# Performance work log

Hardware: AMD Instinct MI355X
Metric: run time of the kernel (lower is better)

Reference implementation:

```python
import jax, jax.numpy as jnp
import numpy as np

SEQ, BATCH = 1024, 2
N_HEAD, D_MODEL = 16, 1024
Q_LORA, KV_LORA = 20, 20
ROPE = D_MODEL // N_HEAD // 2   # 32 qk_rope_head_dim
NOPE = D_MODEL // N_HEAD // 2   # 32 qk_nope_head_dim
V_DIM = D_MODEL // N_HEAD       # 64
N_EXP, HID = 4, 1024            # hidden_dim = d_inner//5 = 5120//5
N_GROUP, TOPK_GROUP, TOP_K = 2, 2, 1
ROUTED_SCALE = 1.0


def setup_inputs() -> dict:
    key = jax.random.key(0)
    ks = jax.random.split(key, 16)
    sc = 0.02
    return {
        'dec_inp': jax.random.normal(ks[0], (SEQ, BATCH, D_MODEL), jnp.float32),
        'wq_a': jax.random.normal(ks[1], (D_MODEL, Q_LORA), jnp.float32) * sc,
        'q_norm_w': jnp.ones((Q_LORA,), jnp.float32),
        'wq_b': jax.random.normal(ks[2], (Q_LORA, N_HEAD * (NOPE + ROPE)), jnp.float32) * sc,
        'wkv_a': jax.random.normal(ks[3], (D_MODEL, KV_LORA + ROPE), jnp.float32) * sc,
        'kv_norm_w': jnp.ones((KV_LORA,), jnp.float32),
        'wkv_b': jax.random.normal(ks[4], (KV_LORA, N_HEAD * (NOPE + V_DIM)), jnp.float32) * sc,
        'wo': jax.random.normal(ks[5], (N_HEAD * V_DIM, D_MODEL), jnp.float32) * sc,
        'gate_w': jax.random.normal(ks[6], (N_EXP, D_MODEL), jnp.float32) * sc,
        'exp_gate': jax.random.normal(ks[7], (N_EXP, D_MODEL, HID), jnp.float32) * sc,
        'exp_up': jax.random.normal(ks[8], (N_EXP, D_MODEL, HID), jnp.float32) * sc,
        'exp_down': jax.random.normal(ks[9], (N_EXP, HID, D_MODEL), jnp.float32) * sc,
        'sh_gate': jax.random.normal(ks[10], (D_MODEL, HID), jnp.float32) * sc,
        'sh_up': jax.random.normal(ks[11], (D_MODEL, HID), jnp.float32) * sc,
        'sh_down': jax.random.normal(ks[12], (HID, D_MODEL), jnp.float32) * sc,
    }


def _rms(x, w, eps=1e-6):
    return x * jax.lax.rsqrt(jnp.mean(x * x, axis=-1, keepdims=True) + eps) * w


def _freqs(seqlen):
    # precompute_freqs_cis(rope_dim * n_head, seqlen): dim = 512 here
    dim = ROPE * N_HEAD
    inv = 1.0 / (10000.0 ** (jnp.arange(0, dim, 2, dtype=jnp.float32) / dim))  # [dim//2]
    ang = jnp.arange(seqlen, dtype=jnp.float32)[:, None] * inv[None, :]       # [s, dim//2]
    ang = ang.reshape(seqlen, N_HEAD, ROPE // 2)
    return jnp.cos(ang), jnp.sin(ang)


def _rope(x, cos, sin):
    # x: [b, s, h, ROPE]; interleaved-pair complex rotation
    b, s, h, _ = x.shape
    xr = x.reshape(b, s, h, ROPE // 2, 2)
    x0, x1 = xr[..., 0], xr[..., 1]
    c = cos[None]  # [1, s, h, ROPE//2]
    sn = sin[None]
    o0 = x0 * c - x1 * sn
    o1 = x0 * sn + x1 * c
    return jnp.stack([o0, o1], axis=-1).reshape(b, s, h, ROPE)


def reference(dec_inp, wq_a, q_norm_w, wq_b, wkv_a, kv_norm_w, wkv_b, wo,
              gate_w, exp_gate, exp_up, exp_down, sh_gate, sh_up, sh_down):
    x = jnp.swapaxes(dec_inp, 0, 1)  # [b, s, d]
    b, s, d = x.shape
    # ---- MLA attention ----
    q = _rms(x @ wq_a, q_norm_w) @ wq_b                       # [b, s, h*(nope+rope)]
    q = q.reshape(b, s, N_HEAD, NOPE + ROPE)
    q_nope, q_pe = q[..., :NOPE], q[..., NOPE:]
    kv = x @ wkv_a                                            # [b, s, kv_lora+rope]
    ckv, k_pe = kv[..., :KV_LORA], kv[..., KV_LORA:]
    kvb = (_rms(ckv, kv_norm_w) @ wkv_b).reshape(b, s, N_HEAD, NOPE + V_DIM)
    k_nope, v = kvb[..., :NOPE], kvb[..., NOPE:]
    cos, sin = _freqs(s)
    q_pe = _rope(q_pe, cos, sin)
    k_pe_h = _rope(jnp.broadcast_to(k_pe[:, :, None, :], (b, s, N_HEAD, ROPE)), cos, sin)
    qf = jnp.concatenate([q_nope, q_pe], axis=-1)             # [b, s, h, 64]
    kf = jnp.concatenate([k_nope, k_pe_h], axis=-1)
    scale = 1.0 / np.sqrt(NOPE + ROPE)
    scores = jnp.einsum('bshd,bthd->bhst', qf, kf) * scale    # mask=None in the source forward
    probs = jax.nn.softmax(scores, axis=-1)
    attn = jnp.einsum('bhst,bthd->bshd', probs, v).reshape(b, s, N_HEAD * V_DIM)
    y = attn @ wo                                             # [b, s, d]
    y = jnp.swapaxes(y, 0, 1)                                 # [s, b, d]
    # ---- DeepSeekMoE (group_limited_greedy, top_k=1, 1 shared expert) ----
    xf = y.reshape(-1, d)                                     # [T, d]
    T = xf.shape[0]
    sc = jax.nn.softmax(xf @ gate_w.T, axis=-1)               # [T, E]
    gsc = sc.reshape(T, N_GROUP, N_EXP // N_GROUP).max(axis=-1)  # [T, n_group]
    _, gidx = jax.lax.top_k(gsc, TOPK_GROUP)
    gmask = jax.nn.one_hot(gidx, N_GROUP, dtype=sc.dtype).sum(axis=1)  # [T, n_group]
    smask = jnp.repeat(gmask, N_EXP // N_GROUP, axis=-1)      # [T, E]
    tw, ti = jax.lax.top_k(jnp.where(smask > 0, sc, 0.0), TOP_K)
    comb = (jax.nn.one_hot(ti, N_EXP, dtype=sc.dtype) * tw[..., None]).sum(axis=1) * ROUTED_SCALE  # [T, E]
    g = jnp.einsum('td,edh->teh', xf, exp_gate)
    u = jnp.einsum('td,edh->teh', xf, exp_up)
    dn = jnp.einsum('teh,ehd->ted', jax.nn.silu(g) * u, exp_down)
    routed = jnp.einsum('ted,te->td', dn, comb)
    shared = (jax.nn.silu(xf @ sh_gate) * (xf @ sh_up)) @ sh_down
    return (routed + shared).reshape(s, b, d)
```

## Files before the change

kernel.cpp:

```cpp
#include <hip/hip_runtime.h>
#include <hip/hip_bf16.h>
#include <math.h>

#define SEQ 1024
#define BATCH 2
#define T 2048
#define DM 1024
#define NH 16
#define NOPE 32
#define HD 64
#define QL 20
#define KVL 20
#define KVA 52
#define HID 1024
#define NEXP 4
#define LSTR 80

typedef short bf16x8 __attribute__((ext_vector_type(8)));
typedef float f32x4 __attribute__((ext_vector_type(4)));
typedef float f32x16 __attribute__((ext_vector_type(16)));
typedef __hip_bfloat16 bf16;

static __device__ __forceinline__ float sigmoidf_(float x) {
    return 1.0f / (1.0f + __expf(-x));
}
static __device__ __forceinline__ unsigned short bfbits(float x) {
    bf16 h = __float2bfloat16(x);
    return *reinterpret_cast<unsigned short*>(&h);
}
static __device__ __forceinline__ unsigned cvt_pk_bf16(float lo, float hi) {
    unsigned r;
    asm("v_cvt_pk_bf16_f32 %0, %1, %2" : "=v"(r) : "v"(lo), "v"(hi));
    return r;
}
static __device__ __forceinline__ void gload16(const bf16* g, char* l) {
    __builtin_amdgcn_global_load_lds(
        (const __attribute__((address_space(1))) unsigned int*)g,
        (__attribute__((address_space(3))) unsigned int*)l, 16, 0, 0);
}
static __device__ __forceinline__ void barrier_() {
    asm volatile("" ::: "memory");
    __builtin_amdgcn_s_barrier();
    asm volatile("" ::: "memory");
}
#define VMWAIT(N) asm volatile("s_waitcnt vmcnt(" #N ")" ::: "memory")

__global__ __launch_bounds__(256) void k_setup(
    const float* __restrict__ wo, const float* __restrict__ sg,
    const float* __restrict__ su, const float* __restrict__ sd,
    const float* __restrict__ eg, const float* __restrict__ eu,
    const float* __restrict__ ed,
    bf16* __restrict__ woT, bf16* __restrict__ sgT, bf16* __restrict__ suT,
    bf16* __restrict__ sdT, bf16* __restrict__ egT, bf16* __restrict__ euT,
    bf16* __restrict__ edT,
    const float* __restrict__ wq_a, const float* __restrict__ wkv_a,
    const float* __restrict__ wq_b, const float* __restrict__ wkv_b,
    bf16* __restrict__ loraT, bf16* __restrict__ wqbT, bf16* __restrict__ wkvbT,
    float* __restrict__ ctab, float* __restrict__ stab)
{
    int z = blockIdx.z;
    int tid = threadIdx.x;
    if (z < 16) {
        __shared__ float tile[32][33];
        const float* in; bf16* out;
        if      (z == 0) { in = wo; out = woT; }
        else if (z == 1) { in = sg; out = sgT; }
        else if (z == 2) { in = su; out = suT; }
        else if (z == 3) { in = sd; out = sdT; }
        else if (z < 8)  { size_t o = (size_t)(z - 4)  * DM * HID; in = eg + o; out = egT + o; }
        else if (z < 12) { size_t o = (size_t)(z - 8)  * DM * HID; in = eu + o; out = euT + o; }
        else             { size_t o = (size_t)(z - 12) * HID * DM; in = ed + o; out = edT + o; }
        int c0 = blockIdx.x * 32, r0 = blockIdx.y * 32;
        int tx = tid & 31, ty = tid >> 5;
        #pragma unroll
        for (int ii = 0; ii < 4; ++ii)
            tile[ty + ii * 8][tx] = in[(size_t)(r0 + ty + ii * 8) * 1024 + c0 + tx];
        __syncthreads();
        int c = tid >> 3, rg = (tid & 7) * 4;
        ushort4 o4;
        o4.x = bfbits(tile[rg + 0][c]);
        o4.y = bfbits(tile[rg + 1][c]);
        o4.z = bfbits(tile[rg + 2][c]);
        o4.w = bfbits(tile[rg + 3][c]);
        *(ushort4*)&out[(size_t)(c0 + c) * 1024 + r0 + rg] = o4;
    } else if (z == 16) {
        int s = blockIdx.y * 32 + blockIdx.x;
        int p = tid;
        float freq = exp2f(-(float)p * (13.287712379549449f / 256.0f));
        float ang = (float)s * freq;
        float sn, cs;
        __sincosf(ang, &sn, &cs);
        ctab[s * 256 + p] = cs;
        stab[s * 256 + p] = sn;
    } else {
        int idx = (blockIdx.y * 32 + blockIdx.x) * 256 + tid;
        if (z == 17) {
            if (idx >= 80 * 1024) return;
            int n = idx >> 10, k = idx & 1023;
            float v = (n < 20) ? wq_a[k * QL + n] : (n < 72 ? wkv_a[k * KVA + (n - 20)] : 0.f);
            loraT[idx] = __float2bfloat16(v);
        } else if (z == 18) {
            if (idx >= 1024 * 32) return;
            int n = idx >> 5, k = idx & 31;
            wqbT[idx] = __float2bfloat16(k < 20 ? wq_b[k * DM + n] : 0.f);
        } else {
            if (idx >= 1536 * 32) return;
            int n = idx >> 5, k = idx & 31;
            wkvbT[idx] = __float2bfloat16(k < 20 ? wkv_b[k * (NH * 96) + n] : 0.f);
        }
    }
}

__global__ __launch_bounds__(256) void k_p1(
    const float* __restrict__ dec, const bf16* __restrict__ loraT,
    float* __restrict__ lora4)
{
    __shared__ __align__(16) char As[128 * LSTR];
    __shared__ __align__(16) char Bs[80 * LSTR];
    const int tid = threadIdx.x;
    const int kz = blockIdx.x;
    const int m0 = blockIdx.y * 128;
    const int lane = tid & 63, wave = tid >> 6;
    const int g = lane >> 4, c = lane & 15;
    f32x4 acc[2][5] = {};
    for (int ks = 0; ks < 16; ++ks) {
        int k0 = kz * 512 + ks * 32;
        __syncthreads();
        #pragma unroll
        for (int pass = 0; pass < 4; ++pass) {
            int row = (tid >> 3) + pass * 32;
            int t = m0 + row;
            int b = t >> 10, s = t & 1023;
            f32x4 v = *(const f32x4*)&dec[(size_t)(s * 2 + b) * DM + k0 + (tid & 7) * 4];
            ushort4 h4;
            h4.x = bfbits(v[0]); h4.y = bfbits(v[1]);
            h4.z = bfbits(v[2]); h4.w = bfbits(v[3]);
            *(ushort4*)&As[row * LSTR + (tid & 7) * 8] = h4;
        }
        if (tid < 160) {
            int row = tid >> 1, hf = tid & 1;
            const bf16* src = &loraT[row * 1024 + k0 + hf * 16];
            *(int4*)&Bs[row * LSTR + hf * 32]      = *(const int4*)&src[0];
            *(int4*)&Bs[row * LSTR + hf * 32 + 16] = *(const int4*)&src[8];
        }
        __syncthreads();
        bf16x8 af[2], bff[5];
        #pragma unroll
        for (int mi = 0; mi < 2; ++mi)
            af[mi] = *(const bf16x8*)&As[(wave * 32 + mi * 16 + c) * LSTR + 16 * g];
        #pragma unroll
        for (int nf = 0; nf < 5; ++nf)
            bff[nf] = *(const bf16x8*)&Bs[(nf * 16 + c) * LSTR + 16 * g];
        #pragma unroll
        for (int mi = 0; mi < 2; ++mi)
            #pragma unroll
            for (int nf = 0; nf < 5; ++nf)
                acc[mi][nf] = __builtin_amdgcn_mfma_f32_16x16x32_bf16(af[mi], bff[nf], acc[mi][nf], 0, 0, 0);
    }
    #pragma unroll
    for (int mi = 0; mi < 2; ++mi)
        #pragma unroll
        for (int nf = 0; nf < 5; ++nf)
            #pragma unroll
            for (int r = 0; r < 4; ++r) {
                int col = nf * 16 + c;
                if (col < 72) {
                    int row = m0 + wave * 32 + mi * 16 + 4 * g + r;
                    lora4[((size_t)kz * T + row) * 72 + col] = acc[mi][nf][r];
                }
            }
}

__global__ __launch_bounds__(256) void k_p2m(
    const float* __restrict__ lora4, const float* __restrict__ qnw,
    const float* __restrict__ kvnw, const float* __restrict__ ctab,
    const float* __restrict__ stab, bf16* __restrict__ nrmq,
    bf16* __restrict__ nrmkv, bf16* __restrict__ kb, int* __restrict__ cnt)
{
    int bid = blockIdx.x, tid = threadIdx.x;
    if (bid == 0 && tid < 16) cnt[tid] = 0;
    {
        int t = bid, p = tid;
        int r = p & 15, h = p >> 4, s = t & (SEQ - 1);
        float y0 = lora4[t * 72 + 40 + 2 * r] + lora4[(size_t)(T + t) * 72 + 40 + 2 * r];
        float y1 = lora4[t * 72 + 41 + 2 * r] + lora4[(size_t)(T + t) * 72 + 41 + 2 * r];
        float cs = ctab[s * 256 + p], sn = stab[s * 256 + p];
        ushort2 pk;
        pk.x = bfbits(y0 * cs - y1 * sn);
        pk.y = bfbits(y0 * sn + y1 * cs);
        *(ushort2*)&kb[(size_t)t * DM + h * HD + NOPE + 2 * r] = pk;
    }
    if (bid < 8) {
        int t = bid * 256 + tid;
        float lq[20], lk[20];
        float ssq = 0.f, ssk = 0.f;
        #pragma unroll
        for (int i = 0; i < 20; ++i) {
            lq[i] = lora4[t * 72 + i] + lora4[(size_t)(T + t) * 72 + i];
            ssq += lq[i] * lq[i];
        }
        #pragma unroll
        for (int i = 0; i < 20; ++i) {
            lk[i] = lora4[t * 72 + 20 + i] + lora4[(size_t)(T + t) * 72 + 20 + i];
            ssk += lk[i] * lk[i];
        }
        float fq = rsqrtf(ssq / 20.f + 1e-6f);
        float fk = rsqrtf(ssk / 20.f + 1e-6f);
        #pragma unroll
        for (int i = 0; i < 32; ++i) {
            nrmq[t * 32 + i]  = __float2bfloat16(i < 20 ? lq[i] * fq * qnw[i]  : 0.f);
            nrmkv[t * 32 + i] = __float2bfloat16(i < 20 ? lk[i] * fk * kvnw[i] : 0.f);
        }
    }
}

__global__ __launch_bounds__(256) void k_p3(
    const bf16* __restrict__ nrmq, const bf16* __restrict__ wqbT,
    const bf16* __restrict__ nrmkv, const bf16* __restrict__ wkvbT,
    const float* __restrict__ ctab, const float* __restrict__ stab,
    bf16* __restrict__ qb, bf16* __restrict__ kb, bf16* __restrict__ vt_g)
{
    const int zq = (blockIdx.z == 0);
    if (zq && blockIdx.x >= 16) return;
    __shared__ __align__(16) char As[128 * LSTR];
    __shared__ __align__(16) char Bs[64 * LSTR];
    const int tid = threadIdx.x;
    const int m0 = blockIdx.y * 128, n0 = blockIdx.x * 64;
    const int lane = tid & 63, wave = tid >> 6;
    const int g = lane >> 4, c = lane & 15;
    const int wm = wave >> 1, wn = wave & 1;
    const bf16* nrm = zq ? nrmq : nrmkv;
    const bf16* wT  = zq ? wqbT : wkvbT;
    {
        int row = tid >> 1, hf = tid & 1;
        const bf16* sa = &nrm[(size_t)(m0 + row) * 32 + hf * 16];
        *(int4*)&As[row * LSTR + hf * 32]      = *(const int4*)&sa[0];
        *(int4*)&As[row * LSTR + hf * 32 + 16] = *(const int4*)&sa[8];
        int brow = tid >> 2;
        *(int4*)&Bs[brow * LSTR + (tid & 3) * 16] = *(const int4*)&wT[(size_t)(n0 + brow) * 32 + (tid & 3) * 8];
    }
    __syncthreads();
    f32x4 acc[4][2] = {};
    bf16x8 af[4], bfr[2];
    #pragma unroll
    for (int mi = 0; mi < 4; ++mi)
        af[mi] = *(const bf16x8*)&As[(wm * 64 + mi * 16 + c) * LSTR + 16 * g];
    #pragma unroll
    for (int ni = 0; ni < 2; ++ni)
        bfr[ni] = *(const bf16x8*)&Bs[(wn * 32 + ni * 16 + c) * LSTR + 16 * g];
    #pragma unroll
    for (int mi = 0; mi < 4; ++mi)
        #pragma unroll
        for (int ni = 0; ni < 2; ++ni)
            acc[mi][ni] = __builtin_amdgcn_mfma_f32_16x16x32_bf16(af[mi], bfr[ni], acc[mi][ni], 0, 0, 0);

    if (zq) {
        #pragma unroll
        for (int mi = 0; mi < 4; ++mi)
            #pragma unroll
            for (int ni = 0; ni < 2; ++ni) {
                #pragma unroll
                for (int r = 0; r < 4; ++r) acc[mi][ni][r] *= 0.18033688f;
                int n = n0 + wn * 32 + ni * 16 + c;
                int w = n & 63;
                if (w < 32) {
                    #pragma unroll
                    for (int r = 0; r < 4; ++r) {
                        int row = m0 + wm * 64 + mi * 16 + 4 * g + r;
                        qb[(size_t)row * DM + n] = __float2bfloat16(acc[mi][ni][r]);
                    }
                } else {
                    int h = n >> 6;
                    int pidx = h * 16 + ((w - 32) >> 1);
                    int odd = w & 1;
                    #pragma unroll
                    for (int r = 0; r < 4; ++r) {
                        int row = m0 + wm * 64 + mi * 16 + 4 * g + r;
                        int s = row & (SEQ - 1);
                        float own = acc[mi][ni][r];
                        float oth = __shfl_xor(own, 1);
                        float cs = ctab[s * 256 + pidx], sn = stab[s * 256 + pidx];
                        float o = odd ? (oth * sn + own * cs) : (own * cs - oth * sn);
                        qb[(size_t)row * DM + n] = __float2bfloat16(o);
                    }
                }
            }
    } else {
        #pragma unroll
        for (int mi = 0; mi < 4; ++mi)
            #pragma unroll
            for (int ni = 0; ni < 2; ++ni) {
                int n = n0 + wn * 32 + ni * 16 + c;
                int h = n / 96, w = n - h * 96;
                int row0 = m0 + wm * 64 + mi * 16 + 4 * g;
                if (w < NOPE) {
                    #pragma unroll
                    for (int r = 0; r < 4; ++r)
                        kb[(size_t)(row0 + r) * DM + h * HD + w] = __float2bfloat16(acc[mi][ni][r]);
                } else {
                    int d = w - NOPE;
                    int b = row0 >> 10, s0 = row0 & (SEQ - 1);
                    ushort4 v4;
                    v4.x = bfbits(acc[mi][ni][0]);
                    v4.y = bfbits(acc[mi][ni][1]);
                    v4.z = bfbits(acc[mi][ni][2]);
                    v4.w = bfbits(acc[mi][ni][3]);
                    *(ushort4*)&vt_g[(((size_t)(b * NH + h) * HD + d) << 10) + s0] = v4;
                }
            }
    }
}

__global__ __launch_bounds__(512) void k_attn(
    const bf16* __restrict__ qb, const bf16* __restrict__ kb,
    const bf16* __restrict__ vt_g, bf16* __restrict__ ab)
{
    __shared__ __align__(16) char stage[2][16384];
    __shared__ float pol[4][32][65];
    __shared__ float mll[4][32][2];

    const int orig = blockIdx.y * 8 + blockIdx.x;
    const int h  = (orig & 7) * 2 + ((orig >> 3) & 1);
    const int qt = orig >> 4;
    const int b = blockIdx.z;
    const int tid = threadIdx.x;
    const int lane = tid & 63, wave = tid >> 6;
    const int l31 = lane & 31, hi = lane >> 5;
    const int sp = wave >> 2, wq = wave & 3;
    const int q0 = qt * 128 + wq * 32;
    char* ks = stage[sp];
    char* vt = stage[sp] + 8192;
    const int ptid = tid & 255;

    bf16x8 qf[4];
    {
        const bf16* qrow = &qb[(size_t)(b * SEQ + q0 + l31) * DM + h * HD + 8 * hi];
        #pragma unroll
        for (int st = 0; st < 4; ++st)
            qf[st] = *(const bf16x8*)&qrow[16 * st];
    }

    f32x16 o0 = {}, o1 = {};
    float m_run = -3.0e38f, l_run = 0.f;
    const size_t vbase = ((size_t)(b * NH + h) * HD) << 10;

    for (int ktl = 0; ktl < 8; ++ktl) {
        const int kt = sp * 8 + ktl;
        __syncthreads();
        #pragma unroll
        for (int ps = 0; ps < 2; ++ps) {
            int row = (ptid >> 3) + ps * 32;
            int col8 = (ptid & 7) * 8;
            int sw = (col8 * 2) ^ ((row & 7) << 4);
            int4 kv4 = *(const int4*)&kb[(size_t)(b * SEQ + kt * 64 + row) * DM + h * HD + col8];
            *(int4*)&ks[row * 128 + sw] = kv4;
            int4 vv4 = *(const int4*)&vt_g[vbase + ((size_t)row << 10) + kt * 64 + col8];
            *(int4*)&vt[row * 128 + sw] = vv4;
        }
        __syncthreads();

        f32x16 sc0 = {}, sc1 = {};
        #pragma unroll
        for (int st = 0; st < 4; ++st) {
            int colb = 32 * st + 16 * hi;
            int r0 = l31;
            bf16x8 kf0 = *(const bf16x8*)&ks[r0 * 128 + (colb ^ ((r0 & 7) << 4))];
            sc0 = __builtin_amdgcn_mfma_f32_32x32x16_bf16(kf0, qf[st], sc0, 0, 0, 0);
            int r1 = 32 + l31;
            bf16x8 kf1 = *(const bf16x8*)&ks[r1 * 128 + (colb ^ ((r1 & 7) << 4))];
            sc1 = __builtin_amdgcn_mfma_f32_32x32x16_bf16(kf1, qf[st], sc1, 0, 0, 0);
        }

        float mt = fmaxf(sc0[0], sc1[0]);
        #pragma unroll
        for (int i = 1; i < 16; ++i) mt = fmaxf(mt, fmaxf(sc0[i], sc1[i]));
        mt = fmaxf(mt, __shfl_xor(mt, 32));

        if (!__all(mt <= m_run + 8.0f)) {
            float m_new = fmaxf(m_run, mt);
            float corr = exp2f(m_run - m_new);
            m_run = m_new;
            l_run *= corr;
            #pragma unroll
            for (int i = 0; i < 16; ++i) { o0[i] *= corr; o1[i] *= corr; }
        }
        float ls = 0.f;
        #pragma unroll
        for (int i = 0; i < 16; ++i) {
            sc0[i] = exp2f(sc0[i] - m_run);
            sc1[i] = exp2f(sc1[i] - m_run);
            ls += sc0[i] + sc1[i];
        }
        ls += __shfl_xor(ls, 32);
        l_run += ls;

        unsigned pk0[8], pk1[8];
        #pragma unroll
        for (int i = 0; i < 8; ++i) {
            pk0[i] = cvt_pk_bf16(sc0[2 * i], sc0[2 * i + 1]);
            pk1[i] = cvt_pk_bf16(sc1[2 * i], sc1[2 * i + 1]);
        }

#define PV_SUB(PK, KK)                                                          \
        {                                                                       \
            _Pragma("unroll")                                                   \
            for (int s = 0; s < 2; ++s) {                                       \
                unsigned sx = hi ? PK[4*s]   : PK[4*s+2];                       \
                unsigned rx = __shfl_xor(sx, 32);                               \
                unsigned sy = hi ? PK[4*s+1] : PK[4*s+3];                       \
                unsigned ry = __shfl_xor(sy, 32);                               \
                int4 bi;                                                        \
                bi.x = hi ? (int)rx : (int)PK[4*s];                             \
                bi.y = hi ? (int)ry : (int)PK[4*s+1];                           \
                bi.z = hi ? (int)PK[4*s+2] : (int)rx;                           \
                bi.w = hi ? (int)PK[4*s+3] : (int)ry;                           \
                bf16x8 bfr = *(bf16x8*)&bi;                                     \
                int cb = (KK) * 64 + 32 * s + 16 * hi;                          \
                {                                                               \
                    int vr = l31;                                               \
                    bf16x8 vf = *(const bf16x8*)&vt[vr * 128 + (cb ^ ((vr & 7) << 4))]; \
                    o0 = __builtin_amdgcn_mfma_f32_32x32x16_bf16(vf, bfr, o0, 0, 0, 0); \
                }                                                               \
                {                                                               \
                    int vr = 32 + l31;                                          \
                    bf16x8 vf = *(const bf16x8*)&vt[vr * 128 + (cb ^ ((vr & 7) << 4))]; \
                    o1 = __builtin_amdgcn_mfma_f32_32x32x16_bf16(vf, bfr, o1, 0, 0, 0); \
                }                                                               \
            }                                                                   \
        }
        PV_SUB(pk0, 0)
        PV_SUB(pk1, 1)
#undef PV_SUB
    }

    if (sp == 1) {
        #pragma unroll
        for (int i = 0; i < 16; ++i) {
            int d = (i & 3) + 8 * (i >> 2) + 4 * hi;
            pol[wq][l31][d]      = o0[i];
            pol[wq][l31][32 + d] = o1[i];
        }
        if (hi == 0) { mll[wq][l31][0] = m_run; mll[wq][l31][1] = l_run; }
    }
    __syncthreads();
    if (sp == 1) return;

    float m_b = mll[wq][l31][0], l_b = mll[wq][l31][1];
    float M = fmaxf(m_run, m_b);
    float wa = exp2f(m_run - M), wb = exp2f(m_b - M);
    float inv = 1.0f / (l_run * wa + l_b * wb);
    #pragma unroll
    for (int i = 0; i < 16; ++i) {
        int d = (i & 3) + 8 * (i >> 2) + 4 * hi;
        o0[i] = (o0[i] * wa + pol[wq][l31][d]      * wb) * inv;
        o1[i] = (o1[i] * wa + pol[wq][l31][32 + d] * wb) * inv;
    }

    char* tb = stage[0] + wq * 8192;
    #pragma unroll
    for (int i = 0; i < 8; ++i) {
        int dbase = 2 * (i & 1) + 8 * (i >> 1) + 4 * hi;
        *(unsigned*)&tb[l31 * 140 + (dbase) * 2]      = cvt_pk_bf16(o0[2 * i], o0[2 * i + 1]);
        *(unsigned*)&tb[l31 * 140 + (32 + dbase) * 2] = cvt_pk_bf16(o1[2 * i], o1[2 * i + 1]);
    }
    __builtin_amdgcn_s_waitcnt(0);
    #pragma unroll
    for (int p = 0; p < 8; ++p) {
        int idx = p * 64 + lane;
        int q = idx >> 4, c8 = idx & 15;
        int2 rv;
        rv.x = *(const int*)&tb[q * 140 + c8 * 8];
        rv.y = *(const int*)&tb[q * 140 + c8 * 8 + 4];
        *(int2*)&ab[(size_t)(b * SEQ + q0 + q) * DM + h * HD + c8 * 4] = rv;
    }
}

__global__ __launch_bounds__(512) void k_mm_plain(
    const bf16* __restrict__ A, const bf16* __restrict__ Bt, bf16* __restrict__ C)
{
    __shared__ __align__(16) char As[2][8192];
    __shared__ __align__(16) char Bs[2][4096];
    const int tid = threadIdx.x;
    const int lane = tid & 63, wave = tid >> 6;
    const int g = lane >> 4, c = lane & 15;
    const int wm = wave >> 1, wn = wave & 1;
    int orig = blockIdx.y * 16 + blockIdx.x;
    int swz = (orig & 7) * 32 + (orig >> 3);
    const int n0 = (swz & 15) * 64, m0 = (swz >> 4) * 128;

    const int ldr = lane >> 2;
    const int ldc = (lane & 3) * 8;
    const bf16* agp = &A[(size_t)(m0 + wave * 16 + ldr) * DM + ldc];
    const bool doB = wave >= 4;
    const bf16* bgp = &Bt[(size_t)(n0 + (wave & 3) * 16 + ldr) * DM + ldc];
    const int aoffL = wave * 1024, boffL = (wave & 3) * 1024;

    f32x4 acc[2][2] = {};
    const int NT = DM / 32;
    gload16(agp, As[0] + aoffL);
    if (doB) gload16(bgp, Bs[0] + boffL);
    for (int k = 0; k < NT; ++k) {
        const int cur = k & 1;
        if (k + 1 < NT) {
            gload16(agp + (k + 1) * 32, As[cur ^ 1] + aoffL);
            if (doB) gload16(bgp + (k + 1) * 32, Bs[cur ^ 1] + boffL);
            if (doB) VMWAIT(2); else VMWAIT(1);
        } else {
            VMWAIT(0);
        }
        barrier_();
        bf16x8 af[2], bfx[2];
        #pragma unroll
        for (int mi = 0; mi < 2; ++mi)
            af[mi] = *(const bf16x8*)&As[cur][(wm * 32 + mi * 16 + c) * 64 + g * 16];
        #pragma unroll
        for (int ni = 0; ni < 2; ++ni)
            bfx[ni] = *(const bf16x8*)&Bs[cur][(wn * 32 + ni * 16 + c) * 64 + g * 16];
        #pragma unroll
        for (int mi = 0; mi < 2; ++mi)
            #pragma unroll
            for (int ni = 0; ni < 2; ++ni)
                acc[mi][ni] = __builtin_amdgcn_mfma_f32_16x16x32_bf16(af[mi], bfx[ni], acc[mi][ni], 0, 0, 0);
        barrier_();
    }
    #pragma unroll
    for (int mi = 0; mi < 2; ++mi)
        #pragma unroll
        for (int ni = 0; ni < 2; ++ni)
            #pragma unroll
            for (int r = 0; r < 4; ++r)
                C[(size_t)(m0 + wm * 32 + mi * 16 + 4 * g + r) * DM + n0 + wn * 32 + ni * 16 + c]
                    = __float2bfloat16(acc[mi][ni][r]);
}

__global__ __launch_bounds__(512) void k_mm_gu_all(
    const bf16* __restrict__ X, const bf16* __restrict__ egT,
    const bf16* __restrict__ euT, const bf16* __restrict__ sgT,
    const bf16* __restrict__ suT, const int* __restrict__ cnt,
    const int* __restrict__ lists, bf16* __restrict__ act_r,
    bf16* __restrict__ act_s)
{
    const int e = blockIdx.z;
    const bool SH = (e == 4);
    const int ntok = SH ? T : cnt[e];
    int orig = blockIdx.y * 16 + blockIdx.x;
    int swz = (orig & 7) * 32 + (orig >> 3);
    const int n0 = (swz & 15) * 64, m0 = (swz >> 4) * 128;
    if (m0 >= ntok) return;
    __shared__ __align__(16) char As[2][8192];
    __shared__ __align__(16) char Bg[2][4096];
    __shared__ __align__(16) char Bu[2][4096];
    __shared__ int rowid[128];
    const int tid = threadIdx.x;
    if (tid < 128) {
        int idx = m0 + tid;
        rowid[tid] = SH ? idx : lists[e * T + (idx < ntok ? idx : ntok - 1)];
    }
    __syncthreads();
    const int lane = tid & 63, wave = tid >> 6;
    const int g = lane >> 4, c = lane & 15;
    const int wm = wave >> 1, wn = wave & 1;
    const bf16* Bge = SH ? sgT : egT + (size_t)e * HID * DM;
    const bf16* Bue = SH ? suT : euT + (size_t)e * HID * DM;
    bf16* act = SH ? act_s : act_r;

    const int ldr = lane >> 2;
    const int ldc = (lane & 3) * 8;
    const int myTok = rowid[wave * 16 + ldr];
    const bf16* agp = &X[(size_t)myTok * DM + ldc];
    const bool isG = wave < 4;
    const bf16* bgp = (isG ? Bge : Bue) + (size_t)(n0 + (wave & 3) * 16 + ldr) * DM + ldc;
    const int aoffL = wave * 1024, boffL = (wave & 3) * 1024;

    f32x4 accg[2][2] = {}, accu[2][2] = {};
    const int NT = DM / 32;
    gload16(agp, As[0] + aoffL);
    gload16(bgp, (isG ? Bg[0] : Bu[0]) + boffL);
    for (int k = 0; k < NT; ++k) {
        const int cur = k & 1;
        if (k + 1 < NT) {
            gload16(agp + (k + 1) * 32, As[cur ^ 1] + aoffL);
            gload16(bgp + (k + 1) * 32, (isG ? Bg[cur ^ 1] : Bu[cur ^ 1]) + boffL);
            VMWAIT(2);
        } else {
            VMWAIT(0);
        }
        barrier_();
        bf16x8 af[2], gf[2], uf[2];
        #pragma unroll
        for (int mi = 0; mi < 2; ++mi)
            af[mi] = *(const bf16x8*)&As[cur][(wm * 32 + mi * 16 + c) * 64 + g * 16];
        #pragma unroll
        for (int ni = 0; ni < 2; ++ni) {
            gf[ni] = *(const bf16x8*)&Bg[cur][(wn * 32 + ni * 16 + c) * 64 + g * 16];
            uf[ni] = *(const bf16x8*)&Bu[cur][(wn * 32 + ni * 16 + c) * 64 + g * 16];
        }
        #pragma unroll
        for (int mi = 0; mi < 2; ++mi)
            #pragma unroll
            for (int ni = 0; ni < 2; ++ni) {
                accg[mi][ni] = __builtin_amdgcn_mfma_f32_16x16x32_bf16(af[mi], gf[ni], accg[mi][ni], 0, 0, 0);
                accu[mi][ni] = __builtin_amdgcn_mfma_f32_16x16x32_bf16(af[mi], uf[ni], accu[mi][ni], 0, 0, 0);
            }
        barrier_();
    }
    #pragma unroll
    for (int mi = 0; mi < 2; ++mi)
        #pragma unroll
        for (int ni = 0; ni < 2; ++ni)
            #pragma unroll
            for (int r = 0; r < 4; ++r) {
                int lr = wm * 32 + mi * 16 + 4 * g + r;
                if (!SH && m0 + lr >= ntok) continue;
                int token = rowid[lr];
                float gv = accg[mi][ni][r], uv = accu[mi][ni][r];
                act[(size_t)token * HID + n0 + wn * 32 + ni * 16 + c] =
                    __float2bfloat16(gv * sigmoidf_(gv) * uv);
            }
}

__global__ __launch_bounds__(512) void k_mm_down_f(
    const bf16* __restrict__ Xr, const bf16* __restrict__ Xs,
    const bf16* __restrict__ edT, const bf16* __restrict__ sdT,
    const int* __restrict__ cnt, const int* __restrict__ lists,
    const float* __restrict__ wtok, float* __restrict__ out)
{
    const int e = blockIdx.z;
    const int ntok = cnt[e];
    int orig = blockIdx.y * 16 + blockIdx.x;
    int swz = (orig & 7) * 32 + (orig >> 3);
    const int n0 = (swz & 15) * 64, m0 = (swz >> 4) * 128;
    if (m0 >= ntok) return;
    __shared__ __align__(16) char Ar[2][8192];
    __shared__ __align__(16) char Az[2][8192];
    __shared__ __align__(16) char Br[2][4096];
    __shared__ __align__(16) char Bz[2][4096];
    __shared__ int rowid[128];
    const int tid = threadIdx.x;
    if (tid < 128) {
        int idx = m0 + tid;
        rowid[tid] = lists[e * T + (idx < ntok ? idx : ntok - 1)];
    }
    __syncthreads();
    const int lane = tid & 63, wave = tid >> 6;
    const int g = lane >> 4, c = lane & 15;
    const int wm = wave >> 1, wn = wave & 1;
    const bf16* Bde = edT + (size_t)e * HID * DM;

    const int ldr = lane >> 2;
    const int ldc = (lane & 3) * 8;
    const int myTok = rowid[wave * 16 + ldr];
    const bf16* agr = &Xr[(size_t)myTok * HID + ldc];
    const bf16* ags = &Xs[(size_t)myTok * HID + ldc];
    const bool isR = wave < 4;
    const bf16* bgp = (isR ? Bde : sdT) + (size_t)(n0 + (wave & 3) * 16 + ldr) * HID + ldc;
    const int aoffL = wave * 1024, boffL = (wave & 3) * 1024;

    f32x4 accr[2][2] = {}, accs[2][2] = {};
    const int NT = HID / 32;
    gload16(agr, Ar[0] + aoffL);
    gload16(ags, Az[0] + aoffL);
    gload16(bgp, (isR ? Br[0] : Bz[0]) + boffL);
    for (int k = 0; k < NT; ++k) {
        const int cur = k & 1;
        if (k + 1 < NT) {
            gload16(agr + (k + 1) * 32, Ar[cur ^ 1] + aoffL);
            gload16(ags + (k + 1) * 32, Az[cur ^ 1] + aoffL);
            gload16(bgp + (k + 1) * 32, (isR ? Br[cur ^ 1] : Bz[cur ^ 1]) + boffL);
            VMWAIT(3);
        } else {
            VMWAIT(0);
        }
        barrier_();
        bf16x8 afr[2], afs[2], bfr[2], bfs[2];
        #pragma unroll
        for (int mi = 0; mi < 2; ++mi) {
            afr[mi] = *(const bf16x8*)&Ar[cur][(wm * 32 + mi * 16 + c) * 64 + g * 16];
            afs[mi] = *(const bf16x8*)&Az[cur][(wm * 32 + mi * 16 + c) * 64 + g * 16];
        }
        #pragma unroll
        for (int ni = 0; ni < 2; ++ni) {
            bfr[ni] = *(const bf16x8*)&Br[cur][(wn * 32 + ni * 16 + c) * 64 + g * 16];
            bfs[ni] = *(const bf16x8*)&Bz[cur][(wn * 32 + ni * 16 + c) * 64 + g * 16];
        }
        #pragma unroll
        for (int mi = 0; mi < 2; ++mi)
            #pragma unroll
            for (int ni = 0; ni < 2; ++ni) {
                accr[mi][ni] = __builtin_amdgcn_mfma_f32_16x16x32_bf16(afr[mi], bfr[ni], accr[mi][ni], 0, 0, 0);
                accs[mi][ni] = __builtin_amdgcn_mfma_f32_16x16x32_bf16(afs[mi], bfs[ni], accs[mi][ni], 0, 0, 0);
            }
        barrier_();
    }
    #pragma unroll
    for (int mi = 0; mi < 2; ++mi)
        #pragma unroll
        for (int ni = 0; ni < 2; ++ni)
            #pragma unroll
            for (int r = 0; r < 4; ++r) {
                int lr = wm * 32 + mi * 16 + 4 * g + r;
                if (m0 + lr >= ntok) continue;
                int token = rowid[lr];
                int bt = token >> 10, st = token & (SEQ - 1);
                size_t oo = (size_t)st * (BATCH * DM) + bt * DM + n0 + wn * 32 + ni * 16 + c;
                out[oo] = accr[mi][ni][r] * wtok[token] + accs[mi][ni][r];
            }
}

__global__ __launch_bounds__(256) void k_gate(
    const bf16* __restrict__ y, const float* __restrict__ gw,
    int* __restrict__ cnt, int* __restrict__ lists, float* __restrict__ wtok)
{
    int warp = threadIdx.x >> 6, lane = threadIdx.x & 63;
    int t = blockIdx.x * 4 + warp;
    float acc[NEXP] = {};
    for (int d = lane; d < DM; d += 64) {
        float xv = __bfloat162float(y[(size_t)t * DM + d]);
        #pragma unroll
        for (int e = 0; e < NEXP; ++e) acc[e] += xv * gw[e * DM + d];
    }
    #pragma unroll
    for (int off = 32; off; off >>= 1)
        #pragma unroll
        for (int e = 0; e < NEXP; ++e) acc[e] += __shfl_xor(acc[e], off);
    if (lane == 0) {
        float mx = fmaxf(fmaxf(acc[0], acc[1]), fmaxf(acc[2], acc[3]));
        float ex[NEXP], ssum = 0.f;
        #pragma unroll
        for (int e = 0; e < NEXP; ++e) { ex[e] = __expf(acc[e] - mx); ssum += ex[e]; }
        int best = 0; float bv = ex[0];
        #pragma unroll
        for (int e = 1; e < NEXP; ++e) if (ex[e] > bv) { bv = ex[e]; best = e; }
        wtok[t] = bv / ssum;
        int pos = atomicAdd(&cnt[best], 1);
        lists[best * T + pos] = t;
    }
}

extern "C" void kernel_launch(void* const* d_in, const int* in_sizes, int n_in,
                              void* d_out, int out_size, void* d_ws, size_t ws_size,
                              hipStream_t stream) {
    (void)in_sizes; (void)n_in; (void)out_size; (void)ws_size;
    const float* dec      = (const float*)d_in[0];
    const float* wq_a     = (const float*)d_in[1];
    const float* q_norm_w = (const float*)d_in[2];
    const float* wq_b     = (const float*)d_in[3];
    const float* wkv_a    = (const float*)d_in[4];
    const float* kv_norm_w= (const float*)d_in[5];
    const float* wkv_b    = (const float*)d_in[6];
    const float* wo       = (const float*)d_in[7];
    const float* gate_w   = (const float*)d_in[8];
    const float* exp_gate = (const float*)d_in[9];
    const float* exp_up   = (const float*)d_in[10];
    const float* exp_down = (const float*)d_in[11];
    const float* sh_gate  = (const float*)d_in[12];
    const float* sh_up    = (const float*)d_in[13];
    const float* sh_down  = (const float*)d_in[14];
    float* out = (float*)d_out;

    char* W = (char*)d_ws;
    bf16* qb   = (bf16*)(W);
    bf16* kb   = (bf16*)(W + (4ull  << 20));
    bf16* vt_g = (bf16*)(W + (8ull  << 20));
    char* SMALL = W + (12ull << 20);
    bf16* ab   = (bf16*)(W + (12ull << 20));
    bf16* woT = (bf16*)(W + (16ull << 20));
    bf16* sgT = (bf16*)(W + (18ull << 20));
    bf16* suT = (bf16*)(W + (20ull << 20));
    bf16* sdT = (bf16*)(W + (22ull << 20));
    bf16* egT = (bf16*)(W + (24ull << 20));
    bf16* euT = (bf16*)(W + (32ull << 20));
    bf16* edT = (bf16*)(W + (40ull << 20));
    int*   cnt   = (int*)(W + (48ull << 20));
    int*   lists = cnt + 16;
    float* wtok  = (float*)(lists + NEXP * T);
    bf16* yb    = qb;
    bf16* act_r = kb;
    bf16* act_s = vt_g;

    float* lora4 = (float*)(SMALL);
    bf16*  loraT = (bf16*) (SMALL + 1179648);
    bf16*  wqbT  = (bf16*) (SMALL + 1343488);
    bf16*  wkvbT = (bf16*) (SMALL + 1409024);
    bf16*  nrmq  = (bf16*) (SMALL + 1507328);
    bf16*  nrmkv = (bf16*) (SMALL + 1638400);
    float* ctab  = (float*)(SMALL + 1769472);
    float* stab  = (float*)(SMALL + 2818048);

    k_setup<<<dim3(32, 32, 20), 256, 0, stream>>>(
        wo, sh_gate, sh_up, sh_down, exp_gate, exp_up, exp_down,
        woT, sgT, suT, sdT, egT, euT, edT,
        wq_a, wkv_a, wq_b, wkv_b, loraT, wqbT, wkvbT, ctab, stab);

    k_p1<<<dim3(2, 16), 256, 0, stream>>>(dec, loraT, lora4);
    k_p2m<<<T, 256, 0, stream>>>(lora4, q_norm_w, kv_norm_w, ctab, stab,
                                 nrmq, nrmkv, kb, cnt);
    k_p3<<<dim3(24, 16, 2), 256, 0, stream>>>(nrmq, wqbT, nrmkv, wkvbT,
                                              ctab, stab, qb, kb, vt_g);

    k_attn<<<dim3(8, 16, BATCH), 512, 0, stream>>>(qb, kb, vt_g, ab);
    k_mm_plain<<<dim3(16, 16), 512, 0, stream>>>(ab, woT, yb);
    k_gate<<<T / 4, 256, 0, stream>>>(yb, gate_w, cnt, lists, wtok);
    k_mm_gu_all<<<dim3(16, 16, NEXP + 1), 512, 0, stream>>>(
        yb, egT, euT, sgT, suT, cnt, lists, act_r, act_s);
    k_mm_down_f<<<dim3(16, 16, NEXP), 512, 0, stream>>>(
        act_r, act_s, edT, sdT, cnt, lists, wtok, out);
}
```

Baseline: 186.6 us.

## Halve attention block size, add MFMA priority, triple-buffer GEMMs dropping trailing barrier

Attention blocks now cover 64 query rows with 256 threads, giving twice as many blocks, and the MFMA sections are wrapped in s_setprio to favour matrix issue. The three GEMM kernels move from double to triple LDS buffers so the trailing per-iteration barrier can be removed, leaving one barrier per k-step. The aim is better latency hiding and higher occupancy for attention, and less synchronisation in the GEMM loops. Risks are the larger LDS footprint lowering GEMM occupancy, and the attention grid remap (blockIdx.y doubled while qt = orig>>4) being correct only if the index arithmetic still covers all query tiles.

```diff
diff --git a/kernel.cpp b/kernel.cpp
--- a/kernel.cpp
+++ b/kernel.cpp
@@ -311,13 +311,13 @@
     }
 }
 
-__global__ __launch_bounds__(512) void k_attn(
+__global__ __launch_bounds__(256) void k_attn(
     const bf16* __restrict__ qb, const bf16* __restrict__ kb,
     const bf16* __restrict__ vt_g, bf16* __restrict__ ab)
 {
     __shared__ __align__(16) char stage[2][16384];
-    __shared__ float pol[4][32][65];
-    __shared__ float mll[4][32][2];
+    __shared__ float pol[2][32][65];
+    __shared__ float mll[2][32][2];
 
     const int orig = blockIdx.y * 8 + blockIdx.x;
     const int h  = (orig & 7) * 2 + ((orig >> 3) & 1);
@@ -326,11 +326,11 @@
     const int tid = threadIdx.x;
     const int lane = tid & 63, wave = tid >> 6;
     const int l31 = lane & 31, hi = lane >> 5;
-    const int sp = wave >> 2, wq = wave & 3;
-    const int q0 = qt * 128 + wq * 32;
+    const int sp = wave >> 1, wq = wave & 1;
+    const int q0 = qt * 64 + wq * 32;
     char* ks = stage[sp];
     char* vt = stage[sp] + 8192;
-    const int ptid = tid & 255;
+    const int ptid = tid & 127;
 
     bf16x8 qf[4];
     {
@@ -348,8 +348,8 @@
         const int kt = sp * 8 + ktl;
         __syncthreads();
         #pragma unroll
-        for (int ps = 0; ps < 2; ++ps) {
-            int row = (ptid >> 3) + ps * 32;
+        for (int ps = 0; ps < 4; ++ps) {
+            int row = (ptid >> 3) + ps * 16;
             int col8 = (ptid & 7) * 8;
             int sw = (col8 * 2) ^ ((row & 7) << 4);
             int4 kv4 = *(const int4*)&kb[(size_t)(b * SEQ + kt * 64 + row) * DM + h * HD + col8];
@@ -360,6 +360,7 @@
         __syncthreads();
 
         f32x16 sc0 = {}, sc1 = {};
+        __builtin_amdgcn_s_setprio(1);
         #pragma unroll
         for (int st = 0; st < 4; ++st) {
             int colb = 32 * st + 16 * hi;
@@ -370,6 +371,7 @@
             bf16x8 kf1 = *(const bf16x8*)&ks[r1 * 128 + (colb ^ ((r1 & 7) << 4))];
             sc1 = __builtin_amdgcn_mfma_f32_32x32x16_bf16(kf1, qf[st], sc1, 0, 0, 0);
         }
+        __builtin_amdgcn_s_setprio(0);
 
         float mt = fmaxf(sc0[0], sc1[0]);
         #pragma unroll
@@ -401,6 +403,7 @@
             pk1[i] = cvt_pk_bf16(sc1[2 * i], sc1[2 * i + 1]);
         }
 
+        __builtin_amdgcn_s_setprio(1);
 #define PV_SUB(PK, KK)                                                          \
         {                                                                       \
             _Pragma("unroll")                                                   \
@@ -431,6 +434,7 @@
         PV_SUB(pk0, 0)
         PV_SUB(pk1, 1)
 #undef PV_SUB
+        __builtin_amdgcn_s_setprio(0);
     }
 
     if (sp == 1) {
@@ -478,8 +482,8 @@
 __global__ __launch_bounds__(512) void k_mm_plain(
     const bf16* __restrict__ A, const bf16* __restrict__ Bt, bf16* __restrict__ C)
 {
-    __shared__ __align__(16) char As[2][8192];
-    __shared__ __align__(16) char Bs[2][4096];
+    __shared__ __align__(16) char As[3][8192];
+    __shared__ __align__(16) char Bs[3][4096];
     const int tid = threadIdx.x;
     const int lane = tid & 63, wave = tid >> 6;
     const int g = lane >> 4, c = lane & 15;
@@ -499,11 +503,12 @@
     const int NT = DM / 32;
     gload16(agp, As[0] + aoffL);
     if (doB) gload16(bgp, Bs[0] + boffL);
+    int cur = 0;
     for (int k = 0; k < NT; ++k) {
-        const int cur = k & 1;
         if (k + 1 < NT) {
-            gload16(agp + (k + 1) * 32, As[cur ^ 1] + aoffL);
-            if (doB) gload16(bgp + (k + 1) * 32, Bs[cur ^ 1] + boffL);
+            int nxt = (cur + 1) % 3;
+            gload16(agp + (k + 1) * 32, As[nxt] + aoffL);
+            if (doB) gload16(bgp + (k + 1) * 32, Bs[nxt] + boffL);
             if (doB) VMWAIT(2); else VMWAIT(1);
         } else {
             VMWAIT(0);
@@ -521,7 +526,7 @@
             #pragma unroll
             for (int ni = 0; ni < 2; ++ni)
                 acc[mi][ni] = __builtin_amdgcn_mfma_f32_16x16x32_bf16(af[mi], bfx[ni], acc[mi][ni], 0, 0, 0);
-        barrier_();
+        cur = (cur + 1) % 3;
     }
     #pragma unroll
     for (int mi = 0; mi < 2; ++mi)
@@ -547,9 +552,9 @@
     int swz = (orig & 7) * 32 + (orig >> 3);
     const int n0 = (swz & 15) * 64, m0 = (swz >> 4) * 128;
     if (m0 >= ntok) return;
-    __shared__ __align__(16) char As[2][8192];
-    __shared__ __align__(16) char Bg[2][4096];
-    __shared__ __align__(16) char Bu[2][4096];
+    __shared__ __align__(16) char As[3][8192];
+    __shared__ __align__(16) char Bg[3][4096];
+    __shared__ __align__(16) char Bu[3][4096];
     __shared__ int rowid[128];
     const int tid = threadIdx.x;
     if (tid < 128) {
@@ -576,11 +581,12 @@
     const int NT = DM / 32;
     gload16(agp, As[0] + aoffL);
     gload16(bgp, (isG ? Bg[0] : Bu[0]) + boffL);
+    int cur = 0;
     for (int k = 0; k < NT; ++k) {
-        const int cur = k & 1;
         if (k + 1 < NT) {
-            gload16(agp + (k + 1) * 32, As[cur ^ 1] + aoffL);
-            gload16(bgp + (k + 1) * 32, (isG ? Bg[cur ^ 1] : Bu[cur ^ 1]) + boffL);
+            int nxt = (cur + 1) % 3;
+            gload16(agp + (k + 1) * 32, As[nxt] + aoffL);
+            gload16(bgp + (k + 1) * 32, (isG ? Bg[nxt] : Bu[nxt]) + boffL);
             VMWAIT(2);
         } else {
             VMWAIT(0);
@@ -602,7 +608,7 @@
                 accg[mi][ni] = __builtin_amdgcn_mfma_f32_16x16x32_bf16(af[mi], gf[ni], accg[mi][ni], 0, 0, 0);
                 accu[mi][ni] = __builtin_amdgcn_mfma_f32_16x16x32_bf16(af[mi], uf[ni], accu[mi][ni], 0, 0, 0);
             }
-        barrier_();
+        cur = (cur + 1) % 3;
     }
     #pragma unroll
     for (int mi = 0; mi < 2; ++mi)
@@ -631,10 +637,10 @@
     int swz = (orig & 7) * 32 + (orig >> 3);
     const int n0 = (swz & 15) * 64, m0 = (swz >> 4) * 128;
     if (m0 >= ntok) return;
-    __shared__ __align__(16) char Ar[2][8192];
-    __shared__ __align__(16) char Az[2][8192];
-    __shared__ __align__(16) char Br[2][4096];
-    __shared__ __align__(16) char Bz[2][4096];
+    __shared__ __align__(16) char Ar[3][8192];
+    __shared__ __align__(16) char Az[3][8192];
+    __shared__ __align__(16) char Br[3][4096];
+    __shared__ __align__(16) char Bz[3][4096];
     __shared__ int rowid[128];
     const int tid = threadIdx.x;
     if (tid < 128) {
@@ -661,12 +667,13 @@
     gload16(agr, Ar[0] + aoffL);
     gload16(ags, Az[0] + aoffL);
     gload16(bgp, (isR ? Br[0] : Bz[0]) + boffL);
+    int cur = 0;
     for (int k = 0; k < NT; ++k) {
-        const int cur = k & 1;
         if (k + 1 < NT) {
-            gload16(agr + (k + 1) * 32, Ar[cur ^ 1] + aoffL);
-            gload16(ags + (k + 1) * 32, Az[cur ^ 1] + aoffL);
-            gload16(bgp + (k + 1) * 32, (isR ? Br[cur ^ 1] : Bz[cur ^ 1]) + boffL);
+            int nxt = (cur + 1) % 3;
+            gload16(agr + (k + 1) * 32, Ar[nxt] + aoffL);
+            gload16(ags + (k + 1) * 32, Az[nxt] + aoffL);
+            gload16(bgp + (k + 1) * 32, (isR ? Br[nxt] : Bz[nxt]) + boffL);
             VMWAIT(3);
         } else {
             VMWAIT(0);
@@ -690,7 +697,7 @@
                 accr[mi][ni] = __builtin_amdgcn_mfma_f32_16x16x32_bf16(afr[mi], bfr[ni], accr[mi][ni], 0, 0, 0);
                 accs[mi][ni] = __builtin_amdgcn_mfma_f32_16x16x32_bf16(afs[mi], bfs[ni], accs[mi][ni], 0, 0, 0);
             }
-        barrier_();
+        cur = (cur + 1) % 3;
     }
     #pragma unroll
     for (int mi = 0; mi < 2; ++mi)
@@ -798,7 +805,7 @@
     k_p3<<<dim3(24, 16, 2), 256, 0, stream>>>(nrmq, wqbT, nrmkv, wkvbT,
                                               ctab, stab, qb, kb, vt_g);
 
-    k_attn<<<dim3(8, 16, BATCH), 512, 0, stream>>>(qb, kb, vt_g, ab);
+    k_attn<<<dim3(8, 32, BATCH), 256, 0, stream>>>(qb, kb, vt_g, ab);
     k_mm_plain<<<dim3(16, 16), 512, 0, stream>>>(ab, woT, yb);
     k_gate<<<T / 4, 256, 0, stream>>>(yb, gate_w, cnt, lists, wtok);
     k_mm_gu_all<<<dim3(16, 16, NEXP + 1), 512, 0, stream>>>(
```

Result: faster. 173.0 us (-7.3%).
